# Kernel optimization log

Measured on AMD Instinct MI355X. Metric: run time of the kernel, lower is better.

## Reference

```python
import jax, jax.numpy as jnp
import numpy as np

B, N, FD, HD, MD, FS, NM = 8, 64, 128, 256, 64, 80, 6
D = HD + MD  # 320: GNN/decoder operating dim (fixes dim bug in original)
H = W = 128

def _mlp2(x, W1, b1, W2, b2):
    return jax.nn.relu(jax.nn.relu(x @ W1 + b1) @ W2 + b2)

def _forward(object_features, object_attributes, perception_features, object_positions,
             enc_W1, enc_b1, enc_W2, enc_b2, conv1_W, conv1_b, conv2_W, conv2_b,
             edge_W1, edge_b1, edge_W2, edge_b2, gru_Wih, gru_Whh, gru_bih, gru_bhh,
             mode_W1, mode_b1, mode_W2, mode_b2, traj_W1, traj_b1, traj_W2, traj_b2):
    # object encoder: [B,N,FD+8] -> [B,N,HD]
    obj_in = jnp.concatenate([object_features, object_attributes], -1)
    emb = _mlp2(obj_in, enc_W1, enc_b1, enc_W2, enc_b2)
    # map encoder (original discards result via random sampler; kept for faithfulness)
    dn = ('NCHW', 'OIHW', 'NCHW')
    m = jax.nn.relu(jax.lax.conv_general_dilated(perception_features, conv1_W, (1, 1), 'SAME', dimension_numbers=dn) + conv1_b[None, :, None, None])
    m = jax.nn.relu(jax.lax.conv_general_dilated(m, conv2_W, (1, 1), 'SAME', dimension_numbers=dn) + conv2_b[None, :, None, None])
    # sample_map_at_positions returns randn in the original; fixed-seed equivalent
    sampled = jax.random.normal(jax.random.key(42), (B, N, MD), dtype=emb.dtype)
    ctx = jnp.concatenate([emb, sampled], -1)  # [B,N,D]
    # Social GNN, fully vectorized over the ego-node loop i:
    rel = object_positions[:, :, None, :] - object_positions[:, None, :, :]  # [B,N,N,2] = pos[i]-pos[j]
    ego = jnp.broadcast_to(ctx[:, :, None, :], (B, N, N, D))
    nbr = jnp.broadcast_to(ctx[:, None, :, :], (B, N, N, D))
    e = _mlp2(jnp.concatenate([ego, nbr, rel], -1), edge_W1, edge_b1, edge_W2, edge_b2)  # [B,N,N,D]
    mask = (1.0 - jnp.eye(N, dtype=e.dtype))[None, :, :, None]
    agg = (e * mask).sum(2) / (N - 1 + 1e-10)  # [B,N,D]
    # GRUCell(input=concat(ctx,agg), hidden=ctx), torch semantics
    x = jnp.concatenate([ctx, agg], -1)  # [B,N,2D]
    gi = x @ gru_Wih + gru_bih
    gh = ctx @ gru_Whh + gru_bhh
    ir, iz, inn = jnp.split(gi, 3, -1)
    hr, hz, hn = jnp.split(gh, 3, -1)
    r = jax.nn.sigmoid(ir + hr)
    z = jax.nn.sigmoid(iz + hz)
    n = jnp.tanh(inn + r * hn)
    h = (1.0 - z) * n + z * ctx  # [B,N,D]
    # multi-modal trajectory decoder
    mode_probs = jax.nn.softmax(jax.nn.relu(h @ mode_W1 + mode_b1) @ mode_W2 + mode_b2, -1)  # [B,N,NM]
    t = jax.nn.relu(jnp.einsum('bnd,mde->bnme', h, traj_W1) + traj_b1)  # [B,N,NM,D]
    traj = jnp.einsum('bnme,mef->bnmf', t, traj_W2) + traj_b2  # [B,N,NM,FS*2]
    traj = traj.reshape(B, N, NM, FS, 2)
    return traj, mode_probs

def setup_inputs() -> dict:
    key = jax.random.key(0)
    ks = jax.random.split(key, 24)
    p = lambda k, shape: jax.random.normal(k, shape, dtype=jnp.float32) * 0.02
    z = lambda *shape: jnp.zeros(shape, dtype=jnp.float32)
    return {
        'object_features': jax.random.normal(ks[0], (B, N, FD), dtype=jnp.float32),
        'object_attributes': jax.random.normal(ks[1], (B, N, 8), dtype=jnp.float32),
        'perception_features': jax.random.normal(ks[2], (B, 256, H, W), dtype=jnp.float32),
        'object_positions': jax.random.normal(ks[3], (B, N, 2), dtype=jnp.float32),
        'enc_W1': p(ks[4], (FD + 8, HD)), 'enc_b1': z(HD),
        'enc_W2': p(ks[5], (HD, HD)), 'enc_b2': z(HD),
        'conv1_W': p(ks[6], (128, 256, 3, 3)), 'conv1_b': z(128),
        'conv2_W': p(ks[7], (64, 128, 3, 3)), 'conv2_b': z(64),
        'edge_W1': p(ks[8], (2 * D + 2, D)), 'edge_b1': z(D),
        'edge_W2': p(ks[9], (D, D)), 'edge_b2': z(D),
        'gru_Wih': p(ks[10], (2 * D, 3 * D)), 'gru_Whh': p(ks[11], (D, 3 * D)),
        'gru_bih': z(3 * D), 'gru_bhh': z(3 * D),
        'mode_W1': p(ks[12], (D, D)), 'mode_b1': z(D),
        'mode_W2': p(ks[13], (D, NM)), 'mode_b2': z(NM),
        'traj_W1': p(ks[14], (NM, D, D)), 'traj_b1': z(NM, D),
        'traj_W2': p(ks[15], (NM, D, FS * 2)), 'traj_b2': z(NM, FS * 2),
    }

def reference(object_features, object_attributes, perception_features, object_positions,
              enc_W1, enc_b1, enc_W2, enc_b2, conv1_W, conv1_b, conv2_W, conv2_b,
              edge_W1, edge_b1, edge_W2, edge_b2, gru_Wih, gru_Whh, gru_bih, gru_bhh,
              mode_W1, mode_b1, mode_W2, mode_b2, traj_W1, traj_b1, traj_W2, traj_b2):
    return _forward(object_features, object_attributes, perception_features, object_positions,
                    enc_W1, enc_b1, enc_W2, enc_b2, conv1_W, conv1_b, conv2_W, conv2_b,
                    edge_W1, edge_b1, edge_W2, edge_b2, gru_Wih, gru_Whh, gru_bih, gru_bhh,
                    mode_W1, mode_b1, mode_W2, mode_b2, traj_W1, traj_b1, traj_W2, traj_b2)
```

## Files before the change

### kernel.cpp

```cpp
#include <hip/hip_runtime.h>


typedef __attribute__((ext_vector_type(8))) short bf16x8;
typedef __attribute__((ext_vector_type(4))) float f32x4;

__device__ __forceinline__ unsigned short f2bf(float x) {
  unsigned u = __float_as_uint(x);
  return (unsigned short)((u + 0x7fffu + ((u >> 16) & 1u)) >> 16);
}

__device__ __forceinline__ void threefry2x32(unsigned k0, unsigned k1,
                                             unsigned& x0, unsigned& x1) {
  const unsigned ks0 = k0, ks1 = k1, ks2 = k0 ^ k1 ^ 0x1BD11BDAu;
  x0 += ks0; x1 += ks1;
#define TFR(r) { x0 += x1; x1 = (x1 << (r)) | (x1 >> (32 - (r))); x1 ^= x0; }
  TFR(13) TFR(15) TFR(26) TFR(6)  x0 += ks1; x1 += ks2 + 1u;
  TFR(17) TFR(29) TFR(16) TFR(24) x0 += ks2; x1 += ks0 + 2u;
  TFR(13) TFR(15) TFR(26) TFR(6)  x0 += ks0; x1 += ks1 + 3u;
  TFR(17) TFR(29) TFR(16) TFR(24) x0 += ks1; x1 += ks2 + 4u;
  TFR(13) TFR(15) TFR(26) TFR(6)  x0 += ks2; x1 += ks0 + 5u;
#undef TFR
}

__device__ __forceinline__ float erfinv_xla(float x) {
  float w = -logf((1.0f - x) * (1.0f + x));
  float p;
  if (w < 5.0f) {
    w = w - 2.5f;
    p = 2.81022636e-08f;
    p = fmaf(p, w, 3.43273939e-07f);
    p = fmaf(p, w, -3.5233877e-06f);
    p = fmaf(p, w, -4.39150654e-06f);
    p = fmaf(p, w, 0.00021858087f);
    p = fmaf(p, w, -0.00125372503f);
    p = fmaf(p, w, -0.00417768164f);
    p = fmaf(p, w, 0.246640727f);
    p = fmaf(p, w, 1.50140941f);
  } else {
    w = sqrtf(w) - 3.0f;
    p = -0.000200214257f;
    p = fmaf(p, w, 0.000100950558f);
    p = fmaf(p, w, 0.00134934322f);
    p = fmaf(p, w, -0.00367342844f);
    p = fmaf(p, w, 0.00573950773f);
    p = fmaf(p, w, -0.0076224613f);
    p = fmaf(p, w, 0.00943887047f);
    p = fmaf(p, w, 1.00167406f);
    p = fmaf(p, w, 2.83297682f);
  }
  return p * x;
}

__device__ __forceinline__ float jax_normal42(unsigned idx) {
  unsigned x0 = 0u, x1 = idx;
  threefry2x32(0u, 42u, x0, x1);
  unsigned bits = x0 ^ x1;
  float f = __uint_as_float((bits >> 9) | 0x3f800000u) - 1.0f;
  const float lo = -0.99999994f;
  float u = fmaxf(lo, f * 2.0f + lo);
  return 1.41421356237f * erfinv_xla(u);
}

__global__ __launch_bounds__(256)
void k_head(const float* __restrict__ W2e, const float* __restrict__ Wih,
            const float* __restrict__ Whh, const float* __restrict__ T1,
            const float* __restrict__ T2, const float* __restrict__ EW1,
            const float* __restrict__ MW1, const float* __restrict__ MW2,
            unsigned short* __restrict__ ub,
            const float* __restrict__ feat, const float* __restrict__ attr,
            const float* __restrict__ eW1, const float* __restrict__ eb1,
            const float* __restrict__ eW2, const float* __restrict__ eb2,
            float* __restrict__ ctx) {
  __shared__ float s_in[4][136];
  __shared__ float s_h1[4][256];
  const int t = threadIdx.x;

  if (blockIdx.x < 1103) {
    const int id = blockIdx.x * 256 + t;
    if (id >= 282240) return;
    if (id >= 281600) {
      const int rem = id - 281600;
      const int g = rem >> 4, n = rem & 15;
      unsigned short v[8];
#pragma unroll
      for (int e = 0; e < 8; ++e) v[e] = (n < 6) ? f2bf(MW2[(g * 8 + e) * 6 + n]) : 0;
      ushort4* d = (ushort4*)&ub[2252800 + (size_t)rem * 8];
      d[0] = make_ushort4(v[0], v[1], v[2], v[3]);
      d[1] = make_ushort4(v[4], v[5], v[6], v[7]);
      return;
    }
    const float* src;
    unsigned short* dst;
    int rem, N;
    if (id < 12800)       { src = W2e; dst = ub;           rem = id;          N = 320; }
    else if (id < 89600)  { src = Wih; dst = ub + 102400;  rem = id - 12800;  N = 960; }
    else if (id < 128000) { src = Whh; dst = ub + 716800;  rem = id - 89600;  N = 960; }
    else if (id < 204800) { src = T1;  dst = ub + 1024000; rem = id - 128000; N = 320; }
    else if (id < 243200) { src = T2;  dst = ub + 1638400; rem = id - 204800; N = 160; }
    else if (id < 268800) { src = EW1; dst = ub + 1945600; rem = id - 243200; N = 320; }
    else                  { src = MW1; dst = ub + 2150400; rem = id - 268800; N = 320; }
    const int g = rem / N, n = rem - g * N;
    const float* s = src + g * 8 * N + n;
    unsigned short v[8];
#pragma unroll
    for (int e = 0; e < 8; ++e) v[e] = f2bf(s[e * N]);
    ushort4* d = (ushort4*)&dst[(size_t)rem * 8];
    d[0] = make_ushort4(v[0], v[1], v[2], v[3]);
    d[1] = make_ushort4(v[4], v[5], v[6], v[7]);
    return;
  }

  const int r0 = (blockIdx.x - 1103) * 4;
  for (int r = 0; r < 4; ++r) {
    if (t < 128)      s_in[r][t] = feat[(r0 + r) * 128 + t];
    else if (t < 136) s_in[r][t] = attr[(r0 + r) * 8 + (t - 128)];
  }
  __syncthreads();
  float acc[4];
#pragma unroll
  for (int r = 0; r < 4; ++r) acc[r] = eb1[t];
  for (int k = 0; k < 136; ++k) {
    const float w = eW1[k * 256 + t];
#pragma unroll
    for (int r = 0; r < 4; ++r) acc[r] = fmaf(s_in[r][k], w, acc[r]);
  }
#pragma unroll
  for (int r = 0; r < 4; ++r) s_h1[r][t] = fmaxf(acc[r], 0.0f);
  __syncthreads();
#pragma unroll
  for (int r = 0; r < 4; ++r) acc[r] = eb2[t];
  for (int k = 0; k < 256; ++k) {
    const float w = eW2[k * 256 + t];
#pragma unroll
    for (int r = 0; r < 4; ++r) acc[r] = fmaf(s_h1[r][k], w, acc[r]);
  }
#pragma unroll
  for (int r = 0; r < 4; ++r) ctx[(r0 + r) * 320 + t] = fmaxf(acc[r], 0.0f);
  if (t < 64) {
    for (int r = 0; r < 4; ++r)
      ctx[(r0 + r) * 320 + 256 + t] = jax_normal42((unsigned)((r0 + r) * 64 + t));
  }
}

__global__ __launch_bounds__(256)
void k_pqM(const float* __restrict__ ctx, const unsigned short* __restrict__ Bf,
           const float* __restrict__ b1, float* __restrict__ P,
           float* __restrict__ Q) {
  __shared__ __align__(16) unsigned short s_c[40 * 16 * 8];
  const int row0 = blockIdx.x * 16;
  const int half = blockIdx.y;
  const int t = threadIdx.x;
#pragma unroll
  for (int it = 0; it < 3; ++it) {
    const int idx = t + it * 256;
    if (idx < 640) {
      const int row = idx / 40, oct = idx - row * 40;
      const float4 v0 = *(const float4*)&ctx[(row0 + row) * 320 + oct * 8];
      const float4 v1 = *(const float4*)&ctx[(row0 + row) * 320 + oct * 8 + 4];
      ushort4* dst = (ushort4*)&s_c[(oct * 16 + row) * 8];
      dst[0] = make_ushort4(f2bf(v0.x), f2bf(v0.y), f2bf(v0.z), f2bf(v0.w));
      dst[1] = make_ushort4(f2bf(v1.x), f2bf(v1.y), f2bf(v1.z), f2bf(v1.w));
    }
  }
  __syncthreads();

  const int w = t >> 6, l = t & 63, lg = l >> 4, lr = l & 15;
  f32x4 acc[5];
#pragma unroll
  for (int u = 0; u < 5; ++u) acc[u] = (f32x4){0.f, 0.f, 0.f, 0.f};
#pragma unroll
  for (int ks = 0; ks < 10; ++ks) {
    const bf16x8 afr = *(const bf16x8*)&s_c[((ks * 4 + lg) * 16 + lr) * 8];
    bf16x8 bfr[5];
#pragma unroll
    for (int u = 0; u < 5; ++u)
      bfr[u] = *(const bf16x8*)&Bf[(((ks * 4 + lg) * 640) + half * 320 +
                                    w * 80 + u * 16 + lr) * 8];
#pragma unroll
    for (int u = 0; u < 5; ++u)
      acc[u] = __builtin_amdgcn_mfma_f32_16x16x32_bf16(afr, bfr[u], acc[u], 0, 0, 0);
  }
#pragma unroll
  for (int u = 0; u < 5; ++u) {
    const int n = w * 80 + u * 16 + lr;
    const float bias = (half == 0) ? b1[n] : 0.0f;
    float* dst = (half == 0) ? P : Q;
#pragma unroll
    for (int r = 0; r < 4; ++r) {
      const int row = row0 + lg * 4 + r;
      dst[row * 320 + n] = acc[u][r] + bias;
    }
  }
}

__global__ __launch_bounds__(256)
void k_edge(const float* __restrict__ P, const float* __restrict__ Q,
            const float* __restrict__ pos, const float* __restrict__ W1,
            const unsigned short* __restrict__ Bf, const float* __restrict__ b2,
            float* __restrict__ agg) {
  __shared__ __align__(16) unsigned short s_A[40 * 64 * 8];
  const int bx = blockIdx.x;
  const int b = bx >> 6, i = bx & 63;
  const int t = threadIdx.x;
  const int w = t >> 6, l = t & 63;

  {
    const float2 pi = *(const float2*)&pos[b * 128 + 2 * i];
    const float* __restrict__ Prow = P + bx * 320;
    const float* __restrict__ w0 = W1 + 640 * 320;
    const float* __restrict__ w1 = W1 + 641 * 320;
#pragma unroll
    for (int it = 0; it < 10; ++it) {
      const int tau = w * 640 + it * 64 + l;
      const int j = tau / 40;
      const int oct = tau - j * 40;
      const int k0 = oct * 8;
      const float2 pj = *(const float2*)&pos[b * 128 + 2 * j];
      const float rx = pi.x - pj.x, ry = pi.y - pj.y;
      const float* __restrict__ Qrow = Q + (b * 64 + j) * 320;
      const float4 q0 = *(const float4*)&Qrow[k0];
      const float4 q1 = *(const float4*)&Qrow[k0 + 4];
      const float4 p0 = *(const float4*)&Prow[k0];
      const float4 p1 = *(const float4*)&Prow[k0 + 4];
      const float4 a0 = *(const float4*)&w0[k0];
      const float4 a1 = *(const float4*)&w0[k0 + 4];
      const float4 c0 = *(const float4*)&w1[k0];
      const float4 c1 = *(const float4*)&w1[k0 + 4];
      float v[8];
      v[0] = fmaf(ry, c0.x, fmaf(rx, a0.x, p0.x + q0.x));
      v[1] = fmaf(ry, c0.y, fmaf(rx, a0.y, p0.y + q0.y));
      v[2] = fmaf(ry, c0.z, fmaf(rx, a0.z, p0.z + q0.z));
      v[3] = fmaf(ry, c0.w, fmaf(rx, a0.w, p0.w + q0.w));
      v[4] = fmaf(ry, c1.x, fmaf(rx, a1.x, p1.x + q1.x));
      v[5] = fmaf(ry, c1.y, fmaf(rx, a1.y, p1.y + q1.y));
      v[6] = fmaf(ry, c1.z, fmaf(rx, a1.z, p1.z + q1.z));
      v[7] = fmaf(ry, c1.w, fmaf(rx, a1.w, p1.w + q1.w));
      unsigned short u[8];
#pragma unroll
      for (int e = 0; e < 8; ++e) u[e] = f2bf(fmaxf(v[e], 0.0f));
      const int swz = ((oct * 64 + j) * 8) ^ ((oct & 7) << 3);
      *(ushort4*)&s_A[swz]     = make_ushort4(u[0], u[1], u[2], u[3]);
      *(ushort4*)&s_A[swz + 4] = make_ushort4(u[4], u[5], u[6], u[7]);
    }
  }
  __syncthreads();

  f32x4 acc[4][5];
#pragma unroll
  for (int mt = 0; mt < 4; ++mt)
#pragma unroll
    for (int u = 0; u < 5; ++u) acc[mt][u] = (f32x4){0.f, 0.f, 0.f, 0.f};

  const int lg = l >> 4, lr = l & 15;
  const unsigned short* __restrict__ Bbase = Bf + (lg * 320 + w * 80 + lr) * 8;

#pragma unroll 2
  for (int ks = 0; ks < 10; ++ks) {
    const int oct = ks * 4 + lg;
    bf16x8 afr[4];
#pragma unroll
    for (int mt = 0; mt < 4; ++mt) {
      const int elem = ((oct * 64 + mt * 16 + lr) * 8) ^ ((oct & 7) << 3);
      afr[mt] = *(const bf16x8*)&s_A[elem];
    }
    bf16x8 bfr[5];
#pragma unroll
    for (int u = 0; u < 5; ++u)
      bfr[u] = *(const bf16x8*)(Bbase + ks * 10240 + u * 128);
#pragma unroll
    for (int mt = 0; mt < 4; ++mt)
#pragma unroll
      for (int u = 0; u < 5; ++u)
        acc[mt][u] = __builtin_amdgcn_mfma_f32_16x16x32_bf16(
            afr[mt], bfr[u], acc[mt][u], 0, 0, 0);
  }

#pragma unroll
  for (int u = 0; u < 5; ++u) {
    const int n = w * 80 + u * 16 + lr;
    const float bias = b2[n];
    float p = 0.0f;
#pragma unroll
    for (int mt = 0; mt < 4; ++mt) {
#pragma unroll
      for (int r = 0; r < 4; ++r) {
        const int j = mt * 16 + lg * 4 + r;
        const float e = fmaxf(acc[mt][u][r] + bias, 0.0f);
        p += (j != i) ? e : 0.0f;
      }
    }
    p += __shfl_xor(p, 16);
    p += __shfl_xor(p, 32);
    if (l < 16) agg[bx * 320 + n] = p * (1.0f / 63.0f);
  }
}

__global__ __launch_bounds__(256)
void k_gruM(const float* __restrict__ ctx, const float* __restrict__ agg,
            const unsigned short* __restrict__ BfI,
            const unsigned short* __restrict__ BfH,
            const float* __restrict__ bih, const float* __restrict__ bhh,
            float* __restrict__ h) {
  __shared__ __align__(16) unsigned short s_x[80 * 16 * 8];
  const int rb = blockIdx.x / 5, db = blockIdx.x % 5;
  const int row0 = rb * 16, d0 = db * 64;
  const int t = threadIdx.x;

#pragma unroll
  for (int it = 0; it < 5; ++it) {
    const int idx = t + it * 256;
    const int row = idx / 80, oct = idx - row * 80;
    float4 v0, v1;
    if (oct < 40) {
      v0 = *(const float4*)&ctx[(row0 + row) * 320 + oct * 8];
      v1 = *(const float4*)&ctx[(row0 + row) * 320 + oct * 8 + 4];
    } else {
      v0 = *(const float4*)&agg[(row0 + row) * 320 + (oct - 40) * 8];
      v1 = *(const float4*)&agg[(row0 + row) * 320 + (oct - 40) * 8 + 4];
    }
    ushort4* dst = (ushort4*)&s_x[(oct * 16 + row) * 8];
    dst[0] = make_ushort4(f2bf(v0.x), f2bf(v0.y), f2bf(v0.z), f2bf(v0.w));
    dst[1] = make_ushort4(f2bf(v1.x), f2bf(v1.y), f2bf(v1.z), f2bf(v1.w));
  }
  __syncthreads();

  const int w = t >> 6, l = t & 63, lg = l >> 4, lr = l & 15;
  const int d = d0 + w * 16 + lr;

  f32x4 accI[3], accH[3];
#pragma unroll
  for (int g = 0; g < 3; ++g) {
    accI[g] = (f32x4){0.f, 0.f, 0.f, 0.f};
    accH[g] = (f32x4){0.f, 0.f, 0.f, 0.f};
  }

#pragma unroll 2
  for (int ks = 0; ks < 20; ++ks) {
    const bf16x8 afr = *(const bf16x8*)&s_x[((ks * 4 + lg) * 16 + lr) * 8];
    bf16x8 bfr[3];
#pragma unroll
    for (int g = 0; g < 3; ++g)
      bfr[g] = *(const bf16x8*)&BfI[((ks * 4 + lg) * 960 + g * 320 + d) * 8];
#pragma unroll
    for (int g = 0; g < 3; ++g)
      accI[g] = __builtin_amdgcn_mfma_f32_16x16x32_bf16(afr, bfr[g], accI[g], 0, 0, 0);
  }
#pragma unroll 2
  for (int ks = 0; ks < 10; ++ks) {
    const bf16x8 afr = *(const bf16x8*)&s_x[((ks * 4 + lg) * 16 + lr) * 8];
    bf16x8 bfr[3];
#pragma unroll
    for (int g = 0; g < 3; ++g)
      bfr[g] = *(const bf16x8*)&BfH[((ks * 4 + lg) * 960 + g * 320 + d) * 8];
#pragma unroll
    for (int g = 0; g < 3; ++g)
      accH[g] = __builtin_amdgcn_mfma_f32_16x16x32_bf16(afr, bfr[g], accH[g], 0, 0, 0);
  }

  const float b_ir = bih[d], b_iz = bih[320 + d], b_in = bih[640 + d];
  const float b_hr = bhh[d], b_hz = bhh[320 + d], b_hn = bhh[640 + d];
#pragma unroll
  for (int r = 0; r < 4; ++r) {
    const int row = row0 + lg * 4 + r;
    const float ir = accI[0][r] + b_ir;
    const float iz = accI[1][r] + b_iz;
    const float inn = accI[2][r] + b_in;
    const float hr = accH[0][r] + b_hr;
    const float hz = accH[1][r] + b_hz;
    const float hn = accH[2][r] + b_hn;
    const float rr = 1.0f / (1.0f + expf(-(ir + hr)));
    const float zz = 1.0f / (1.0f + expf(-(iz + hz)));
    const float nn = tanhf(fmaf(rr, hn, inn));
    const float c = ctx[row * 320 + d];
    h[row * 320 + d] = (1.0f - zz) * nn + zz * c;
  }
}

__global__ __launch_bounds__(256)
void k_tail(const float* __restrict__ h, const unsigned short* __restrict__ MB1,
            const float* __restrict__ mb1, const unsigned short* __restrict__ MB2,
            const float* __restrict__ mb2, const unsigned short* __restrict__ TB1,
            const float* __restrict__ tb1, const unsigned short* __restrict__ TB2,
            const float* __restrict__ tb2, float* __restrict__ out) {
  __shared__ __align__(16) unsigned short s_buf[20480];
  __shared__ float s_l[32][6];
  const int t = threadIdx.x;
  const int w = t >> 6, l = t & 63, lg = l >> 4, lr = l & 15;

  if (blockIdx.x < 16) {
    unsigned short* s_h = s_buf;
    unsigned short* s_t = s_buf + 10240;
    const int row0 = blockIdx.x * 32;
#pragma unroll
    for (int it = 0; it < 5; ++it) {
      const int idx = t + it * 256;
      const int row = idx / 40, oct = idx - row * 40;
      const float4 v0 = *(const float4*)&h[(row0 + row) * 320 + oct * 8];
      const float4 v1 = *(const float4*)&h[(row0 + row) * 320 + oct * 8 + 4];
      ushort4* dst = (ushort4*)&s_h[(oct * 32 + row) * 8];
      dst[0] = make_ushort4(f2bf(v0.x), f2bf(v0.y), f2bf(v0.z), f2bf(v0.w));
      dst[1] = make_ushort4(f2bf(v1.x), f2bf(v1.y), f2bf(v1.z), f2bf(v1.w));
    }
    __syncthreads();

    f32x4 acc1[2][5];
#pragma unroll
    for (int mt = 0; mt < 2; ++mt)
#pragma unroll
      for (int u = 0; u < 5; ++u) acc1[mt][u] = (f32x4){0.f, 0.f, 0.f, 0.f};
#pragma unroll
    for (int ks = 0; ks < 10; ++ks) {
      bf16x8 afr[2];
#pragma unroll
      for (int mt = 0; mt < 2; ++mt)
        afr[mt] = *(const bf16x8*)&s_h[(((ks * 4 + lg) * 32) + mt * 16 + lr) * 8];
      bf16x8 bfr[5];
#pragma unroll
      for (int u = 0; u < 5; ++u)
        bfr[u] = *(const bf16x8*)&MB1[((ks * 4 + lg) * 320 + w * 80 + u * 16 + lr) * 8];
#pragma unroll
      for (int mt = 0; mt < 2; ++mt)
#pragma unroll
        for (int u = 0; u < 5; ++u)
          acc1[mt][u] = __builtin_amdgcn_mfma_f32_16x16x32_bf16(
              afr[mt], bfr[u], acc1[mt][u], 0, 0, 0);
    }
#pragma unroll
    for (int u = 0; u < 5; ++u) {
      const int n = w * 80 + u * 16 + lr;
      const float bias = mb1[n];
#pragma unroll
      for (int mt = 0; mt < 2; ++mt) {
#pragma unroll
        for (int r = 0; r < 4; ++r) {
          const int row = mt * 16 + lg * 4 + r;
          s_t[((n >> 3) * 32 + row) * 8 + (n & 7)] =
              f2bf(fmaxf(acc1[mt][u][r] + bias, 0.0f));
        }
      }
    }
    __syncthreads();

    if (w < 2) {
      f32x4 acc2 = (f32x4){0.f, 0.f, 0.f, 0.f};
#pragma unroll
      for (int ks = 0; ks < 10; ++ks) {
        const bf16x8 afr = *(const bf16x8*)&s_t[(((ks * 4 + lg) * 32) + w * 16 + lr) * 8];
        const bf16x8 bfr = *(const bf16x8*)&MB2[((ks * 4 + lg) * 16 + lr) * 8];
        acc2 = __builtin_amdgcn_mfma_f32_16x16x32_bf16(afr, bfr, acc2, 0, 0, 0);
      }
      if (lr < 6) {
#pragma unroll
        for (int r = 0; r < 4; ++r)
          s_l[w * 16 + lg * 4 + r][lr] = acc2[r] + mb2[lr];
      }
    }
    __syncthreads();

    if (t < 32) {
      float v[6];
#pragma unroll
      for (int q = 0; q < 6; ++q) v[q] = s_l[t][q];
      float mx = v[0];
#pragma unroll
      for (int q = 1; q < 6; ++q) mx = fmaxf(mx, v[q]);
      float sum = 0.0f;
#pragma unroll
      for (int q = 0; q < 6; ++q) { v[q] = expf(v[q] - mx); sum += v[q]; }
      const float inv = 1.0f / sum;
#pragma unroll
      for (int q = 0; q < 6; ++q) out[491520 + (row0 + t) * 6 + q] = v[q] * inv;
    }
    return;
  }

  const int idx0 = blockIdx.x - 16;
  const int m = idx0 >> 5, rb = idx0 & 31;
  unsigned short* s_h = s_buf;
  unsigned short* s_t = s_buf + 5120;
  const int row0 = rb * 16;

#pragma unroll
  for (int it = 0; it < 3; ++it) {
    const int idx = t + it * 256;
    if (idx < 640) {
      const int row = idx / 40, oct = idx - row * 40;
      const float4 v0 = *(const float4*)&h[(row0 + row) * 320 + oct * 8];
      const float4 v1 = *(const float4*)&h[(row0 + row) * 320 + oct * 8 + 4];
      ushort4* dst = (ushort4*)&s_h[(oct * 16 + row) * 8];
      dst[0] = make_ushort4(f2bf(v0.x), f2bf(v0.y), f2bf(v0.z), f2bf(v0.w));
      dst[1] = make_ushort4(f2bf(v1.x), f2bf(v1.y), f2bf(v1.z), f2bf(v1.w));
    }
  }
  __syncthreads();

  f32x4 acc1[5];
#pragma unroll
  for (int u = 0; u < 5; ++u) acc1[u] = (f32x4){0.f, 0.f, 0.f, 0.f};
  const unsigned short* __restrict__ B1m = TB1 + m * 102400;
#pragma unroll
  for (int ks = 0; ks < 10; ++ks) {
    const bf16x8 afr = *(const bf16x8*)&s_h[((ks * 4 + lg) * 16 + lr) * 8];
    bf16x8 bfr[5];
#pragma unroll
    for (int u = 0; u < 5; ++u)
      bfr[u] = *(const bf16x8*)&B1m[((ks * 4 + lg) * 320 + w * 80 + u * 16 + lr) * 8];
#pragma unroll
    for (int u = 0; u < 5; ++u)
      acc1[u] = __builtin_amdgcn_mfma_f32_16x16x32_bf16(afr, bfr[u], acc1[u], 0, 0, 0);
  }
#pragma unroll
  for (int u = 0; u < 5; ++u) {
    const int n = w * 80 + u * 16 + lr;
    const float bias = tb1[m * 320 + n];
#pragma unroll
    for (int r = 0; r < 4; ++r) {
      const int row = lg * 4 + r;
      s_t[((n >> 3) * 16 + row) * 8 + (n & 7)] =
          f2bf(fmaxf(acc1[u][r] + bias, 0.0f));
    }
  }
  __syncthreads();

  const int nb = (w == 0) ? 0 : (w == 1) ? 3 : (w == 2) ? 6 : 7;
  f32x4 acc2[3];
#pragma unroll
  for (int u = 0; u < 3; ++u) acc2[u] = (f32x4){0.f, 0.f, 0.f, 0.f};
  const unsigned short* __restrict__ B2m = TB2 + m * 51200;
#pragma unroll
  for (int ks = 0; ks < 10; ++ks) {
    const bf16x8 afr = *(const bf16x8*)&s_t[((ks * 4 + lg) * 16 + lr) * 8];
    bf16x8 bfr[3];
#pragma unroll
    for (int u = 0; u < 3; ++u)
      bfr[u] = *(const bf16x8*)&B2m[((ks * 4 + lg) * 160 + (nb + u) * 16 + lr) * 8];
#pragma unroll
    for (int u = 0; u < 3; ++u)
      acc2[u] = __builtin_amdgcn_mfma_f32_16x16x32_bf16(afr, bfr[u], acc2[u], 0, 0, 0);
  }
#pragma unroll
  for (int u = 0; u < 3; ++u) {
    const int n = (nb + u) * 16 + lr;
    const float bias = tb2[m * 160 + n];
#pragma unroll
    for (int r = 0; r < 4; ++r) {
      const int row = row0 + lg * 4 + r;
      out[(row * 6 + m) * 160 + n] = acc2[u][r] + bias;
    }
  }
}

extern "C" void kernel_launch(void* const* d_in, const int* in_sizes, int n_in,
                              void* d_out, int out_size, void* d_ws, size_t ws_size,
                              hipStream_t stream) {
  (void)in_sizes; (void)n_in; (void)out_size; (void)ws_size;
  const float* feat  = (const float*)d_in[0];
  const float* attr  = (const float*)d_in[1];
  const float* pos   = (const float*)d_in[3];
  const float* encW1 = (const float*)d_in[4];
  const float* encb1 = (const float*)d_in[5];
  const float* encW2 = (const float*)d_in[6];
  const float* encb2 = (const float*)d_in[7];
  const float* edgW1 = (const float*)d_in[12];
  const float* edgb1 = (const float*)d_in[13];
  const float* edgW2 = (const float*)d_in[14];
  const float* edgb2 = (const float*)d_in[15];
  const float* Wih   = (const float*)d_in[16];
  const float* Whh   = (const float*)d_in[17];
  const float* bih   = (const float*)d_in[18];
  const float* bhh   = (const float*)d_in[19];
  const float* mW1   = (const float*)d_in[20];
  const float* mb1   = (const float*)d_in[21];
  const float* mW2   = (const float*)d_in[22];
  const float* mb2   = (const float*)d_in[23];
  const float* tW1   = (const float*)d_in[24];
  const float* tb1   = (const float*)d_in[25];
  const float* tW2   = (const float*)d_in[26];
  const float* tb2   = (const float*)d_in[27];

  float* out = (float*)d_out;
  float* ws  = (float*)d_ws;
  float* ctx  = ws;
  float* P    = ws + 163840;
  float* Q    = ws + 327680;
  float* agg  = ws + 491520;
  float* hbuf = ws + 655360;
  unsigned short* ub = (unsigned short*)(ws + 819200);
  unsigned short* W2bf  = ub;
  unsigned short* WihBf = ub + 102400;
  unsigned short* WhhBf = ub + 716800;
  unsigned short* T1bf  = ub + 1024000;
  unsigned short* T2bf  = ub + 1638400;
  unsigned short* EW1bf = ub + 1945600;
  unsigned short* MW1bf = ub + 2150400;
  unsigned short* MW2bf = ub + 2252800;

  k_head<<<1231, 256, 0, stream>>>(edgW2, Wih, Whh, tW1, tW2, edgW1, mW1, mW2, ub,
                                   feat, attr, encW1, encb1, encW2, encb2, ctx);
  k_pqM<<<dim3(32, 2), 256, 0, stream>>>(ctx, EW1bf, edgb1, P, Q);
  k_edge<<<512, 256, 0, stream>>>(P, Q, pos, edgW1, W2bf, edgb2, agg);
  k_gruM<<<160, 256, 0, stream>>>(ctx, agg, WihBf, WhhBf, bih, bhh, hbuf);
  k_tail<<<208, 256, 0, stream>>>(hbuf, MW1bf, mb1, MW2bf, mb2,
                                  T1bf, tb1, T2bf, tb2, out);
}
```

Baseline: 78.35 us.

## Fuse all stages into one persistent kernel with software grid barriers

Merges the five kernel launches into a single 256-block persistent kernel, with stages separated by an atomic-counter grid barrier, and adds a memset to reset the barrier. This removes per-launch overhead and the gaps between launches. In exchange, each stage now runs on at most 256 blocks, so the weight conversion and edge work loop over more items per block. The barrier spin-waits also add cost, and the scheme assumes all 256 blocks are co-resident.

```diff
diff --git a/kernel.cpp b/kernel.cpp
--- a/kernel.cpp
+++ b/kernel.cpp
@@ -61,23 +61,55 @@
   return 1.41421356237f * erfinv_xla(u);
 }
 
+__device__ __forceinline__ void gridbar(unsigned* bar, unsigned target) {
+  __syncthreads();
+  if (threadIdx.x == 0) {
+    __threadfence();
+    if (atomicAdd(&bar[0], 1u) == 255u) {
+      bar[0] = 0u;
+      __threadfence();
+      atomicAdd(&bar[1], 1u);
+    } else {
+      while (atomicAdd(&bar[1], 0u) < target) { __builtin_amdgcn_s_sleep(2); }
+    }
+    __threadfence();
+  }
+  __syncthreads();
+}
+
 __global__ __launch_bounds__(256)
-void k_head(const float* __restrict__ W2e, const float* __restrict__ Wih,
-            const float* __restrict__ Whh, const float* __restrict__ T1,
-            const float* __restrict__ T2, const float* __restrict__ EW1,
-            const float* __restrict__ MW1, const float* __restrict__ MW2,
-            unsigned short* __restrict__ ub,
-            const float* __restrict__ feat, const float* __restrict__ attr,
-            const float* __restrict__ eW1, const float* __restrict__ eb1,
-            const float* __restrict__ eW2, const float* __restrict__ eb2,
-            float* __restrict__ ctx) {
-  __shared__ float s_in[4][136];
-  __shared__ float s_h1[4][256];
+void k_fused(const float* __restrict__ W2e, const float* __restrict__ Wih,
+             const float* __restrict__ Whh, const float* __restrict__ T1,
+             const float* __restrict__ T2, const float* __restrict__ EW1,
+             const float* __restrict__ MW1, const float* __restrict__ MW2,
+             unsigned short* __restrict__ ub,
+             const float* __restrict__ feat, const float* __restrict__ attr,
+             const float* __restrict__ eW1, const float* __restrict__ eb1,
+             const float* __restrict__ eW2, const float* __restrict__ eb2,
+             const float* __restrict__ pos, const float* __restrict__ edgW1,
+             const float* __restrict__ edgb1, const float* __restrict__ edgb2,
+             const float* __restrict__ bih, const float* __restrict__ bhh,
+             const float* __restrict__ mb1, const float* __restrict__ mb2,
+             const float* __restrict__ tb1, const float* __restrict__ tb2,
+             float* __restrict__ ctx, float* __restrict__ P,
+             float* __restrict__ Q, float* __restrict__ agg,
+             float* __restrict__ hbuf, float* __restrict__ out,
+             unsigned* __restrict__ bar) {
+  __shared__ __align__(16) unsigned char smem[41728];
+  const int bid = blockIdx.x;
   const int t = threadIdx.x;
-
-  if (blockIdx.x < 1103) {
-    const int id = blockIdx.x * 256 + t;
-    if (id >= 282240) return;
+  const int w = t >> 6, l = t & 63, lg = (l >> 4), lr = l & 15;
+
+  const unsigned short* W2bf  = ub;
+  const unsigned short* WihBf = ub + 102400;
+  const unsigned short* WhhBf = ub + 716800;
+  const unsigned short* T1bf  = ub + 1024000;
+  const unsigned short* T2bf  = ub + 1638400;
+  const unsigned short* EW1bf = ub + 1945600;
+  const unsigned short* MW1bf = ub + 2150400;
+  const unsigned short* MW2bf = ub + 2252800;
+
+  for (int id = bid * 256 + t; id < 282240; id += 65536) {
     if (id >= 281600) {
       const int rem = id - 281600;
       const int g = rem >> 4, n = rem & 15;
@@ -87,7 +119,7 @@
       ushort4* d = (ushort4*)&ub[2252800 + (size_t)rem * 8];
       d[0] = make_ushort4(v[0], v[1], v[2], v[3]);
       d[1] = make_ushort4(v[4], v[5], v[6], v[7]);
-      return;
+      continue;
     }
     const float* src;
     unsigned short* dst;
@@ -107,296 +139,268 @@
     ushort4* d = (ushort4*)&dst[(size_t)rem * 8];
     d[0] = make_ushort4(v[0], v[1], v[2], v[3]);
     d[1] = make_ushort4(v[4], v[5], v[6], v[7]);
-    return;
-  }
-
-  const int r0 = (blockIdx.x - 1103) * 4;
-  for (int r = 0; r < 4; ++r) {
-    if (t < 128)      s_in[r][t] = feat[(r0 + r) * 128 + t];
-    else if (t < 136) s_in[r][t] = attr[(r0 + r) * 8 + (t - 128)];
-  }
-  __syncthreads();
-  float acc[4];
-#pragma unroll
-  for (int r = 0; r < 4; ++r) acc[r] = eb1[t];
-  for (int k = 0; k < 136; ++k) {
-    const float w = eW1[k * 256 + t];
-#pragma unroll
-    for (int r = 0; r < 4; ++r) acc[r] = fmaf(s_in[r][k], w, acc[r]);
-  }
-#pragma unroll
-  for (int r = 0; r < 4; ++r) s_h1[r][t] = fmaxf(acc[r], 0.0f);
-  __syncthreads();
-#pragma unroll
-  for (int r = 0; r < 4; ++r) acc[r] = eb2[t];
-  for (int k = 0; k < 256; ++k) {
-    const float w = eW2[k * 256 + t];
-#pragma unroll
-    for (int r = 0; r < 4; ++r) acc[r] = fmaf(s_h1[r][k], w, acc[r]);
-  }
-#pragma unroll
-  for (int r = 0; r < 4; ++r) ctx[(r0 + r) * 320 + t] = fmaxf(acc[r], 0.0f);
-  if (t < 64) {
-    for (int r = 0; r < 4; ++r)
-      ctx[(r0 + r) * 320 + 256 + t] = jax_normal42((unsigned)((r0 + r) * 64 + t));
-  }
-}
-
-__global__ __launch_bounds__(256)
-void k_pqM(const float* __restrict__ ctx, const unsigned short* __restrict__ Bf,
-           const float* __restrict__ b1, float* __restrict__ P,
-           float* __restrict__ Q) {
-  __shared__ __align__(16) unsigned short s_c[40 * 16 * 8];
-  const int row0 = blockIdx.x * 16;
-  const int half = blockIdx.y;
-  const int t = threadIdx.x;
-#pragma unroll
-  for (int it = 0; it < 3; ++it) {
-    const int idx = t + it * 256;
-    if (idx < 640) {
-      const int row = idx / 40, oct = idx - row * 40;
-      const float4 v0 = *(const float4*)&ctx[(row0 + row) * 320 + oct * 8];
-      const float4 v1 = *(const float4*)&ctx[(row0 + row) * 320 + oct * 8 + 4];
-      ushort4* dst = (ushort4*)&s_c[(oct * 16 + row) * 8];
+  }
+
+  {
+    float (*s_in)[136] = (float (*)[136])smem;
+    float (*s_h1)[256] = (float (*)[256])(smem + 2 * 136 * 4);
+    const int r0 = bid * 2;
+    for (int r = 0; r < 2; ++r) {
+      if (t < 128)      s_in[r][t] = feat[(r0 + r) * 128 + t];
+      else if (t < 136) s_in[r][t] = attr[(r0 + r) * 8 + (t - 128)];
+    }
+    __syncthreads();
+    float acc[2];
+#pragma unroll
+    for (int r = 0; r < 2; ++r) acc[r] = eb1[t];
+    for (int k = 0; k < 136; ++k) {
+      const float ww = eW1[k * 256 + t];
+#pragma unroll
+      for (int r = 0; r < 2; ++r) acc[r] = fmaf(s_in[r][k], ww, acc[r]);
+    }
+#pragma unroll
+    for (int r = 0; r < 2; ++r) s_h1[r][t] = fmaxf(acc[r], 0.0f);
+    __syncthreads();
+#pragma unroll
+    for (int r = 0; r < 2; ++r) acc[r] = eb2[t];
+    for (int k = 0; k < 256; ++k) {
+      const float ww = eW2[k * 256 + t];
+#pragma unroll
+      for (int r = 0; r < 2; ++r) acc[r] = fmaf(s_h1[r][k], ww, acc[r]);
+    }
+#pragma unroll
+    for (int r = 0; r < 2; ++r) ctx[(r0 + r) * 320 + t] = fmaxf(acc[r], 0.0f);
+    if (t < 64) {
+      for (int r = 0; r < 2; ++r)
+        ctx[(r0 + r) * 320 + 256 + t] = jax_normal42((unsigned)((r0 + r) * 64 + t));
+    }
+  }
+  gridbar(bar, 1);
+
+  if (bid < 64) {
+    unsigned short* s_c = (unsigned short*)smem;
+    const int row0 = (bid >> 1) * 16;
+    const int half = bid & 1;
+#pragma unroll
+    for (int it = 0; it < 3; ++it) {
+      const int idx = t + it * 256;
+      if (idx < 640) {
+        const int row = idx / 40, oct = idx - row * 40;
+        const float4 v0 = *(const float4*)&ctx[(row0 + row) * 320 + oct * 8];
+        const float4 v1 = *(const float4*)&ctx[(row0 + row) * 320 + oct * 8 + 4];
+        ushort4* dst = (ushort4*)&s_c[(oct * 16 + row) * 8];
+        dst[0] = make_ushort4(f2bf(v0.x), f2bf(v0.y), f2bf(v0.z), f2bf(v0.w));
+        dst[1] = make_ushort4(f2bf(v1.x), f2bf(v1.y), f2bf(v1.z), f2bf(v1.w));
+      }
+    }
+    __syncthreads();
+    f32x4 acc[5];
+#pragma unroll
+    for (int u = 0; u < 5; ++u) acc[u] = (f32x4){0.f, 0.f, 0.f, 0.f};
+#pragma unroll
+    for (int ks = 0; ks < 10; ++ks) {
+      const bf16x8 afr = *(const bf16x8*)&s_c[((ks * 4 + lg) * 16 + lr) * 8];
+      bf16x8 bfr[5];
+#pragma unroll
+      for (int u = 0; u < 5; ++u)
+        bfr[u] = *(const bf16x8*)&EW1bf[(((ks * 4 + lg) * 640) + half * 320 +
+                                        w * 80 + u * 16 + lr) * 8];
+#pragma unroll
+      for (int u = 0; u < 5; ++u)
+        acc[u] = __builtin_amdgcn_mfma_f32_16x16x32_bf16(afr, bfr[u], acc[u], 0, 0, 0);
+    }
+#pragma unroll
+    for (int u = 0; u < 5; ++u) {
+      const int n = w * 80 + u * 16 + lr;
+      const float bias = (half == 0) ? edgb1[n] : 0.0f;
+      float* dst = (half == 0) ? P : Q;
+#pragma unroll
+      for (int r = 0; r < 4; ++r) {
+        const int row = row0 + lg * 4 + r;
+        dst[row * 320 + n] = acc[u][r] + bias;
+      }
+    }
+  }
+  gridbar(bar, 2);
+
+  {
+    unsigned short* s_A = (unsigned short*)smem;
+    for (int sub = 0; sub < 2; ++sub) {
+      const int bx = bid * 2 + sub;
+      const int b = bx >> 6, i = bx & 63;
+      {
+        const float2 pi = *(const float2*)&pos[b * 128 + 2 * i];
+        const float* __restrict__ Prow = P + bx * 320;
+        const float* __restrict__ w0 = edgW1 + 640 * 320;
+        const float* __restrict__ w1 = edgW1 + 641 * 320;
+#pragma unroll
+        for (int it = 0; it < 10; ++it) {
+          const int tau = w * 640 + it * 64 + l;
+          const int j = tau / 40;
+          const int oct = tau - j * 40;
+          const int k0 = oct * 8;
+          const float2 pj = *(const float2*)&pos[b * 128 + 2 * j];
+          const float rx = pi.x - pj.x, ry = pi.y - pj.y;
+          const float* __restrict__ Qrow = Q + (b * 64 + j) * 320;
+          const float4 q0 = *(const float4*)&Qrow[k0];
+          const float4 q1 = *(const float4*)&Qrow[k0 + 4];
+          const float4 p0 = *(const float4*)&Prow[k0];
+          const float4 p1 = *(const float4*)&Prow[k0 + 4];
+          const float4 a0 = *(const float4*)&w0[k0];
+          const float4 a1 = *(const float4*)&w0[k0 + 4];
+          const float4 c0 = *(const float4*)&w1[k0];
+          const float4 c1 = *(const float4*)&w1[k0 + 4];
+          float v[8];
+          v[0] = fmaf(ry, c0.x, fmaf(rx, a0.x, p0.x + q0.x));
+          v[1] = fmaf(ry, c0.y, fmaf(rx, a0.y, p0.y + q0.y));
+          v[2] = fmaf(ry, c0.z, fmaf(rx, a0.z, p0.z + q0.z));
+          v[3] = fmaf(ry, c0.w, fmaf(rx, a0.w, p0.w + q0.w));
+          v[4] = fmaf(ry, c1.x, fmaf(rx, a1.x, p1.x + q1.x));
+          v[5] = fmaf(ry, c1.y, fmaf(rx, a1.y, p1.y + q1.y));
+          v[6] = fmaf(ry, c1.z, fmaf(rx, a1.z, p1.z + q1.z));
+          v[7] = fmaf(ry, c1.w, fmaf(rx, a1.w, p1.w + q1.w));
+          unsigned short u[8];
+#pragma unroll
+          for (int e = 0; e < 8; ++e) u[e] = f2bf(fmaxf(v[e], 0.0f));
+          const int swz = ((oct * 64 + j) * 8) ^ ((oct & 7) << 3);
+          *(ushort4*)&s_A[swz]     = make_ushort4(u[0], u[1], u[2], u[3]);
+          *(ushort4*)&s_A[swz + 4] = make_ushort4(u[4], u[5], u[6], u[7]);
+        }
+      }
+      __syncthreads();
+
+      f32x4 acc[4][5];
+#pragma unroll
+      for (int mt = 0; mt < 4; ++mt)
+#pragma unroll
+        for (int u = 0; u < 5; ++u) acc[mt][u] = (f32x4){0.f, 0.f, 0.f, 0.f};
+      const unsigned short* __restrict__ Bbase = W2bf + (lg * 320 + w * 80 + lr) * 8;
+#pragma unroll 2
+      for (int ks = 0; ks < 10; ++ks) {
+        const int oct = ks * 4 + lg;
+        bf16x8 afr[4];
+#pragma unroll
+        for (int mt = 0; mt < 4; ++mt) {
+          const int elem = ((oct * 64 + mt * 16 + lr) * 8) ^ ((oct & 7) << 3);
+          afr[mt] = *(const bf16x8*)&s_A[elem];
+        }
+        bf16x8 bfr[5];
+#pragma unroll
+        for (int u = 0; u < 5; ++u)
+          bfr[u] = *(const bf16x8*)(Bbase + ks * 10240 + u * 128);
+#pragma unroll
+        for (int mt = 0; mt < 4; ++mt)
+#pragma unroll
+          for (int u = 0; u < 5; ++u)
+            acc[mt][u] = __builtin_amdgcn_mfma_f32_16x16x32_bf16(
+                afr[mt], bfr[u], acc[mt][u], 0, 0, 0);
+      }
+
+#pragma unroll
+      for (int u = 0; u < 5; ++u) {
+        const int n = w * 80 + u * 16 + lr;
+        const float bias = edgb2[n];
+        float p = 0.0f;
+#pragma unroll
+        for (int mt = 0; mt < 4; ++mt) {
+#pragma unroll
+          for (int r = 0; r < 4; ++r) {
+            const int j = mt * 16 + lg * 4 + r;
+            const float e = fmaxf(acc[mt][u][r] + bias, 0.0f);
+            p += (j != i) ? e : 0.0f;
+          }
+        }
+        p += __shfl_xor(p, 16);
+        p += __shfl_xor(p, 32);
+        if (l < 16) agg[bx * 320 + n] = p * (1.0f / 63.0f);
+      }
+      __syncthreads();
+    }
+  }
+  gridbar(bar, 3);
+
+  if (bid < 160) {
+    unsigned short* s_x = (unsigned short*)smem;
+    const int rb = bid / 5, db = bid % 5;
+    const int row0 = rb * 16, d0 = db * 64;
+#pragma unroll
+    for (int it = 0; it < 5; ++it) {
+      const int idx = t + it * 256;
+      const int row = idx / 80, oct = idx - row * 80;
+      float4 v0, v1;
+      if (oct < 40) {
+        v0 = *(const float4*)&ctx[(row0 + row) * 320 + oct * 8];
+        v1 = *(const float4*)&ctx[(row0 + row) * 320 + oct * 8 + 4];
+      } else {
+        v0 = *(const float4*)&agg[(row0 + row) * 320 + (oct - 40) * 8];
+        v1 = *(const float4*)&agg[(row0 + row) * 320 + (oct - 40) * 8 + 4];
+      }
+      ushort4* dst = (ushort4*)&s_x[(oct * 16 + row) * 8];
       dst[0] = make_ushort4(f2bf(v0.x), f2bf(v0.y), f2bf(v0.z), f2bf(v0.w));
       dst[1] = make_ushort4(f2bf(v1.x), f2bf(v1.y), f2bf(v1.z), f2bf(v1.w));
     }
-  }
-  __syncthreads();
-
-  const int w = t >> 6, l = t & 63, lg = l >> 4, lr = l & 15;
-  f32x4 acc[5];
-#pragma unroll
-  for (int u = 0; u < 5; ++u) acc[u] = (f32x4){0.f, 0.f, 0.f, 0.f};
-#pragma unroll
-  for (int ks = 0; ks < 10; ++ks) {
-    const bf16x8 afr = *(const bf16x8*)&s_c[((ks * 4 + lg) * 16 + lr) * 8];
-    bf16x8 bfr[5];
-#pragma unroll
-    for (int u = 0; u < 5; ++u)
-      bfr[u] = *(const bf16x8*)&Bf[(((ks * 4 + lg) * 640) + half * 320 +
-                                    w * 80 + u * 16 + lr) * 8];
-#pragma unroll
-    for (int u = 0; u < 5; ++u)
-      acc[u] = __builtin_amdgcn_mfma_f32_16x16x32_bf16(afr, bfr[u], acc[u], 0, 0, 0);
-  }
-#pragma unroll
-  for (int u = 0; u < 5; ++u) {
-    const int n = w * 80 + u * 16 + lr;
-    const float bias = (half == 0) ? b1[n] : 0.0f;
-    float* dst = (half == 0) ? P : Q;
+    __syncthreads();
+
+    const int d = d0 + w * 16 + lr;
+    f32x4 accI[3], accH[3];
+#pragma unroll
+    for (int g = 0; g < 3; ++g) {
+      accI[g] = (f32x4){0.f, 0.f, 0.f, 0.f};
+      accH[g] = (f32x4){0.f, 0.f, 0.f, 0.f};
+    }
+#pragma unroll 2
+    for (int ks = 0; ks < 20; ++ks) {
+      const bf16x8 afr = *(const bf16x8*)&s_x[((ks * 4 + lg) * 16 + lr) * 8];
+      bf16x8 bfr[3];
+#pragma unroll
+      for (int g = 0; g < 3; ++g)
+        bfr[g] = *(const bf16x8*)&WihBf[((ks * 4 + lg) * 960 + g * 320 + d) * 8];
+#pragma unroll
+      for (int g = 0; g < 3; ++g)
+        accI[g] = __builtin_amdgcn_mfma_f32_16x16x32_bf16(afr, bfr[g], accI[g], 0, 0, 0);
+    }
+#pragma unroll 2
+    for (int ks = 0; ks < 10; ++ks) {
+      const bf16x8 afr = *(const bf16x8*)&s_x[((ks * 4 + lg) * 16 + lr) * 8];
+      bf16x8 bfr[3];
+#pragma unroll
+      for (int g = 0; g < 3; ++g)
+        bfr[g] = *(const bf16x8*)&WhhBf[((ks * 4 + lg) * 960 + g * 320 + d) * 8];
+#pragma unroll
+      for (int g = 0; g < 3; ++g)
+        accH[g] = __builtin_amdgcn_mfma_f32_16x16x32_bf16(afr, bfr[g], accH[g], 0, 0, 0);
+    }
+    const float b_ir = bih[d], b_iz = bih[320 + d], b_in = bih[640 + d];
+    const float b_hr = bhh[d], b_hz = bhh[320 + d], b_hn = bhh[640 + d];
 #pragma unroll
     for (int r = 0; r < 4; ++r) {
       const int row = row0 + lg * 4 + r;
-      dst[row * 320 + n] = acc[u][r] + bias;
-    }
-  }
-}
-
-__global__ __launch_bounds__(256)
-void k_edge(const float* __restrict__ P, const float* __restrict__ Q,
-            const float* __restrict__ pos, const float* __restrict__ W1,
-            const unsigned short* __restrict__ Bf, const float* __restrict__ b2,
-            float* __restrict__ agg) {
-  __shared__ __align__(16) unsigned short s_A[40 * 64 * 8];
-  const int bx = blockIdx.x;
-  const int b = bx >> 6, i = bx & 63;
-  const int t = threadIdx.x;
-  const int w = t >> 6, l = t & 63;
-
-  {
-    const float2 pi = *(const float2*)&pos[b * 128 + 2 * i];
-    const float* __restrict__ Prow = P + bx * 320;
-    const float* __restrict__ w0 = W1 + 640 * 320;
-    const float* __restrict__ w1 = W1 + 641 * 320;
-#pragma unroll
-    for (int it = 0; it < 10; ++it) {
-      const int tau = w * 640 + it * 64 + l;
-      const int j = tau / 40;
-      const int oct = tau - j * 40;
-      const int k0 = oct * 8;
-      const float2 pj = *(const float2*)&pos[b * 128 + 2 * j];
-      const float rx = pi.x - pj.x, ry = pi.y - pj.y;
-      const float* __restrict__ Qrow = Q + (b * 64 + j) * 320;
-      const float4 q0 = *(const float4*)&Qrow[k0];
-      const float4 q1 = *(const float4*)&Qrow[k0 + 4];
-      const float4 p0 = *(const float4*)&Prow[k0];
-      const float4 p1 = *(const float4*)&Prow[k0 + 4];
-      const float4 a0 = *(const float4*)&w0[k0];
-      const float4 a1 = *(const float4*)&w0[k0 + 4];
-      const float4 c0 = *(const float4*)&w1[k0];
-      const float4 c1 = *(const float4*)&w1[k0 + 4];
-      float v[8];
-      v[0] = fmaf(ry, c0.x, fmaf(rx, a0.x, p0.x + q0.x));
-      v[1] = fmaf(ry, c0.y, fmaf(rx, a0.y, p0.y + q0.y));
-      v[2] = fmaf(ry, c0.z, fmaf(rx, a0.z, p0.z + q0.z));
-      v[3] = fmaf(ry, c0.w, fmaf(rx, a0.w, p0.w + q0.w));
-      v[4] = fmaf(ry, c1.x, fmaf(rx, a1.x, p1.x + q1.x));
-      v[5] = fmaf(ry, c1.y, fmaf(rx, a1.y, p1.y + q1.y));
-      v[6] = fmaf(ry, c1.z, fmaf(rx, a1.z, p1.z + q1.z));
-      v[7] = fmaf(ry, c1.w, fmaf(rx, a1.w, p1.w + q1.w));
-      unsigned short u[8];
-#pragma unroll
-      for (int e = 0; e < 8; ++e) u[e] = f2bf(fmaxf(v[e], 0.0f));
-      const int swz = ((oct * 64 + j) * 8) ^ ((oct & 7) << 3);
-      *(ushort4*)&s_A[swz]     = make_ushort4(u[0], u[1], u[2], u[3]);
-      *(ushort4*)&s_A[swz + 4] = make_ushort4(u[4], u[5], u[6], u[7]);
-    }
-  }
-  __syncthreads();
-
-  f32x4 acc[4][5];
-#pragma unroll
-  for (int mt = 0; mt < 4; ++mt)
-#pragma unroll
-    for (int u = 0; u < 5; ++u) acc[mt][u] = (f32x4){0.f, 0.f, 0.f, 0.f};
-
-  const int lg = l >> 4, lr = l & 15;
-  const unsigned short* __restrict__ Bbase = Bf + (lg * 320 + w * 80 + lr) * 8;
-
-#pragma unroll 2
-  for (int ks = 0; ks < 10; ++ks) {
-    const int oct = ks * 4 + lg;
-    bf16x8 afr[4];
-#pragma unroll
-    for (int mt = 0; mt < 4; ++mt) {
-      const int elem = ((oct * 64 + mt * 16 + lr) * 8) ^ ((oct & 7) << 3);
-      afr[mt] = *(const bf16x8*)&s_A[elem];
-    }
-    bf16x8 bfr[5];
-#pragma unroll
-    for (int u = 0; u < 5; ++u)
-      bfr[u] = *(const bf16x8*)(Bbase + ks * 10240 + u * 128);
-#pragma unroll
-    for (int mt = 0; mt < 4; ++mt)
-#pragma unroll
-      for (int u = 0; u < 5; ++u)
-        acc[mt][u] = __builtin_amdgcn_mfma_f32_16x16x32_bf16(
-            afr[mt], bfr[u], acc[mt][u], 0, 0, 0);
-  }
-
-#pragma unroll
-  for (int u = 0; u < 5; ++u) {
-    const int n = w * 80 + u * 16 + lr;
-    const float bias = b2[n];
-    float p = 0.0f;
-#pragma unroll
-    for (int mt = 0; mt < 4; ++mt) {
-#pragma unroll
-      for (int r = 0; r < 4; ++r) {
-        const int j = mt * 16 + lg * 4 + r;
-        const float e = fmaxf(acc[mt][u][r] + bias, 0.0f);
-        p += (j != i) ? e : 0.0f;
-      }
-    }
-    p += __shfl_xor(p, 16);
-    p += __shfl_xor(p, 32);
-    if (l < 16) agg[bx * 320 + n] = p * (1.0f / 63.0f);
-  }
-}
-
-__global__ __launch_bounds__(256)
-void k_gruM(const float* __restrict__ ctx, const float* __restrict__ agg,
-            const unsigned short* __restrict__ BfI,
-            const unsigned short* __restrict__ BfH,
-            const float* __restrict__ bih, const float* __restrict__ bhh,
-            float* __restrict__ h) {
-  __shared__ __align__(16) unsigned short s_x[80 * 16 * 8];
-  const int rb = blockIdx.x / 5, db = blockIdx.x % 5;
-  const int row0 = rb * 16, d0 = db * 64;
-  const int t = threadIdx.x;
-
-#pragma unroll
-  for (int it = 0; it < 5; ++it) {
-    const int idx = t + it * 256;
-    const int row = idx / 80, oct = idx - row * 80;
-    float4 v0, v1;
-    if (oct < 40) {
-      v0 = *(const float4*)&ctx[(row0 + row) * 320 + oct * 8];
-      v1 = *(const float4*)&ctx[(row0 + row) * 320 + oct * 8 + 4];
-    } else {
-      v0 = *(const float4*)&agg[(row0 + row) * 320 + (oct - 40) * 8];
-      v1 = *(const float4*)&agg[(row0 + row) * 320 + (oct - 40) * 8 + 4];
-    }
-    ushort4* dst = (ushort4*)&s_x[(oct * 16 + row) * 8];
-    dst[0] = make_ushort4(f2bf(v0.x), f2bf(v0.y), f2bf(v0.z), f2bf(v0.w));
-    dst[1] = make_ushort4(f2bf(v1.x), f2bf(v1.y), f2bf(v1.z), f2bf(v1.w));
-  }
-  __syncthreads();
-
-  const int w = t >> 6, l = t & 63, lg = l >> 4, lr = l & 15;
-  const int d = d0 + w * 16 + lr;
-
-  f32x4 accI[3], accH[3];
-#pragma unroll
-  for (int g = 0; g < 3; ++g) {
-    accI[g] = (f32x4){0.f, 0.f, 0.f, 0.f};
-    accH[g] = (f32x4){0.f, 0.f, 0.f, 0.f};
-  }
-
-#pragma unroll 2
-  for (int ks = 0; ks < 20; ++ks) {
-    const bf16x8 afr = *(const bf16x8*)&s_x[((ks * 4 + lg) * 16 + lr) * 8];
-    bf16x8 bfr[3];
-#pragma unroll
-    for (int g = 0; g < 3; ++g)
-      bfr[g] = *(const bf16x8*)&BfI[((ks * 4 + lg) * 960 + g * 320 + d) * 8];
-#pragma unroll
-    for (int g = 0; g < 3; ++g)
-      accI[g] = __builtin_amdgcn_mfma_f32_16x16x32_bf16(afr, bfr[g], accI[g], 0, 0, 0);
-  }
-#pragma unroll 2
-  for (int ks = 0; ks < 10; ++ks) {
-    const bf16x8 afr = *(const bf16x8*)&s_x[((ks * 4 + lg) * 16 + lr) * 8];
-    bf16x8 bfr[3];
-#pragma unroll
-    for (int g = 0; g < 3; ++g)
-      bfr[g] = *(const bf16x8*)&BfH[((ks * 4 + lg) * 960 + g * 320 + d) * 8];
-#pragma unroll
-    for (int g = 0; g < 3; ++g)
-      accH[g] = __builtin_amdgcn_mfma_f32_16x16x32_bf16(afr, bfr[g], accH[g], 0, 0, 0);
-  }
-
-  const float b_ir = bih[d], b_iz = bih[320 + d], b_in = bih[640 + d];
-  const float b_hr = bhh[d], b_hz = bhh[320 + d], b_hn = bhh[640 + d];
-#pragma unroll
-  for (int r = 0; r < 4; ++r) {
-    const int row = row0 + lg * 4 + r;
-    const float ir = accI[0][r] + b_ir;
-    const float iz = accI[1][r] + b_iz;
-    const float inn = accI[2][r] + b_in;
-    const float hr = accH[0][r] + b_hr;
-    const float hz = accH[1][r] + b_hz;
-    const float hn = accH[2][r] + b_hn;
-    const float rr = 1.0f / (1.0f + expf(-(ir + hr)));
-    const float zz = 1.0f / (1.0f + expf(-(iz + hz)));
-    const float nn = tanhf(fmaf(rr, hn, inn));
-    const float c = ctx[row * 320 + d];
-    h[row * 320 + d] = (1.0f - zz) * nn + zz * c;
-  }
-}
-
-__global__ __launch_bounds__(256)
-void k_tail(const float* __restrict__ h, const unsigned short* __restrict__ MB1,
-            const float* __restrict__ mb1, const unsigned short* __restrict__ MB2,
-            const float* __restrict__ mb2, const unsigned short* __restrict__ TB1,
-            const float* __restrict__ tb1, const unsigned short* __restrict__ TB2,
-            const float* __restrict__ tb2, float* __restrict__ out) {
-  __shared__ __align__(16) unsigned short s_buf[20480];
-  __shared__ float s_l[32][6];
-  const int t = threadIdx.x;
-  const int w = t >> 6, l = t & 63, lg = l >> 4, lr = l & 15;
-
-  if (blockIdx.x < 16) {
-    unsigned short* s_h = s_buf;
-    unsigned short* s_t = s_buf + 10240;
-    const int row0 = blockIdx.x * 32;
+      const float ir = accI[0][r] + b_ir;
+      const float iz = accI[1][r] + b_iz;
+      const float inn = accI[2][r] + b_in;
+      const float hr = accH[0][r] + b_hr;
+      const float hz = accH[1][r] + b_hz;
+      const float hn = accH[2][r] + b_hn;
+      const float rr = 1.0f / (1.0f + expf(-(ir + hr)));
+      const float zz = 1.0f / (1.0f + expf(-(iz + hz)));
+      const float nn = tanhf(fmaf(rr, hn, inn));
+      const float c = ctx[row * 320 + d];
+      hbuf[row * 320 + d] = (1.0f - zz) * nn + zz * c;
+    }
+  }
+  gridbar(bar, 4);
+
+  if (bid < 16) {
+    unsigned short* s_h = (unsigned short*)smem;
+    unsigned short* s_t = (unsigned short*)(smem + 20480);
+    float (*s_l)[6] = (float (*)[6])(smem + 40960);
+    const int row0 = bid * 32;
 #pragma unroll
     for (int it = 0; it < 5; ++it) {
       const int idx = t + it * 256;
       const int row = idx / 40, oct = idx - row * 40;
-      const float4 v0 = *(const float4*)&h[(row0 + row) * 320 + oct * 8];
-      const float4 v1 = *(const float4*)&h[(row0 + row) * 320 + oct * 8 + 4];
+      const float4 v0 = *(const float4*)&hbuf[(row0 + row) * 320 + oct * 8];
+      const float4 v1 = *(const float4*)&hbuf[(row0 + row) * 320 + oct * 8 + 4];
       ushort4* dst = (ushort4*)&s_h[(oct * 32 + row) * 8];
       dst[0] = make_ushort4(f2bf(v0.x), f2bf(v0.y), f2bf(v0.z), f2bf(v0.w));
       dst[1] = make_ushort4(f2bf(v1.x), f2bf(v1.y), f2bf(v1.z), f2bf(v1.w));
@@ -417,7 +421,7 @@
       bf16x8 bfr[5];
 #pragma unroll
       for (int u = 0; u < 5; ++u)
-        bfr[u] = *(const bf16x8*)&MB1[((ks * 4 + lg) * 320 + w * 80 + u * 16 + lr) * 8];
+        bfr[u] = *(const bf16x8*)&MW1bf[((ks * 4 + lg) * 320 + w * 80 + u * 16 + lr) * 8];
 #pragma unroll
       for (int mt = 0; mt < 2; ++mt)
 #pragma unroll
@@ -446,7 +450,7 @@
 #pragma unroll
       for (int ks = 0; ks < 10; ++ks) {
         const bf16x8 afr = *(const bf16x8*)&s_t[(((ks * 4 + lg) * 32) + w * 16 + lr) * 8];
-        const bf16x8 bfr = *(const bf16x8*)&MB2[((ks * 4 + lg) * 16 + lr) * 8];
+        const bf16x8 bfr = *(const bf16x8*)&MW2bf[((ks * 4 + lg) * 16 + lr) * 8];
         acc2 = __builtin_amdgcn_mfma_f32_16x16x32_bf16(afr, bfr, acc2, 0, 0, 0);
       }
       if (lr < 6) {
@@ -471,81 +475,79 @@
 #pragma unroll
       for (int q = 0; q < 6; ++q) out[491520 + (row0 + t) * 6 + q] = v[q] * inv;
     }
-    return;
-  }
-
-  const int idx0 = blockIdx.x - 16;
-  const int m = idx0 >> 5, rb = idx0 & 31;
-  unsigned short* s_h = s_buf;
-  unsigned short* s_t = s_buf + 5120;
-  const int row0 = rb * 16;
-
-#pragma unroll
-  for (int it = 0; it < 3; ++it) {
-    const int idx = t + it * 256;
-    if (idx < 640) {
-      const int row = idx / 40, oct = idx - row * 40;
-      const float4 v0 = *(const float4*)&h[(row0 + row) * 320 + oct * 8];
-      const float4 v1 = *(const float4*)&h[(row0 + row) * 320 + oct * 8 + 4];
-      ushort4* dst = (ushort4*)&s_h[(oct * 16 + row) * 8];
-      dst[0] = make_ushort4(f2bf(v0.x), f2bf(v0.y), f2bf(v0.z), f2bf(v0.w));
-      dst[1] = make_ushort4(f2bf(v1.x), f2bf(v1.y), f2bf(v1.z), f2bf(v1.w));
-    }
-  }
-  __syncthreads();
-
-  f32x4 acc1[5];
-#pragma unroll
-  for (int u = 0; u < 5; ++u) acc1[u] = (f32x4){0.f, 0.f, 0.f, 0.f};
-  const unsigned short* __restrict__ B1m = TB1 + m * 102400;
-#pragma unroll
-  for (int ks = 0; ks < 10; ++ks) {
-    const bf16x8 afr = *(const bf16x8*)&s_h[((ks * 4 + lg) * 16 + lr) * 8];
-    bf16x8 bfr[5];
-#pragma unroll
-    for (int u = 0; u < 5; ++u)
-      bfr[u] = *(const bf16x8*)&B1m[((ks * 4 + lg) * 320 + w * 80 + u * 16 + lr) * 8];
-#pragma unroll
-    for (int u = 0; u < 5; ++u)
-      acc1[u] = __builtin_amdgcn_mfma_f32_16x16x32_bf16(afr, bfr[u], acc1[u], 0, 0, 0);
-  }
-#pragma unroll
-  for (int u = 0; u < 5; ++u) {
-    const int n = w * 80 + u * 16 + lr;
-    const float bias = tb1[m * 320 + n];
-#pragma unroll
-    for (int r = 0; r < 4; ++r) {
-      const int row = lg * 4 + r;
-      s_t[((n >> 3) * 16 + row) * 8 + (n & 7)] =
-          f2bf(fmaxf(acc1[u][r] + bias, 0.0f));
-    }
-  }
-  __syncthreads();
-
-  const int nb = (w == 0) ? 0 : (w == 1) ? 3 : (w == 2) ? 6 : 7;
-  f32x4 acc2[3];
-#pragma unroll
-  for (int u = 0; u < 3; ++u) acc2[u] = (f32x4){0.f, 0.f, 0.f, 0.f};
-  const unsigned short* __restrict__ B2m = TB2 + m * 51200;
-#pragma unroll
-  for (int ks = 0; ks < 10; ++ks) {
-    const bf16x8 afr = *(const bf16x8*)&s_t[((ks * 4 + lg) * 16 + lr) * 8];
-    bf16x8 bfr[3];
-#pragma unroll
-    for (int u = 0; u < 3; ++u)
-      bfr[u] = *(const bf16x8*)&B2m[((ks * 4 + lg) * 160 + (nb + u) * 16 + lr) * 8];
-#pragma unroll
-    for (int u = 0; u < 3; ++u)
-      acc2[u] = __builtin_amdgcn_mfma_f32_16x16x32_bf16(afr, bfr[u], acc2[u], 0, 0, 0);
-  }
-#pragma unroll
-  for (int u = 0; u < 3; ++u) {
-    const int n = (nb + u) * 16 + lr;
-    const float bias = tb2[m * 160 + n];
-#pragma unroll
-    for (int r = 0; r < 4; ++r) {
-      const int row = row0 + lg * 4 + r;
-      out[(row * 6 + m) * 160 + n] = acc2[u][r] + bias;
+  } else if (bid < 208) {
+    const int idx0 = bid - 16;
+    const int m = idx0 >> 5, rb = idx0 & 31;
+    unsigned short* s_h = (unsigned short*)smem;
+    unsigned short* s_t = (unsigned short*)(smem + 10240);
+    const int row0 = rb * 16;
+#pragma unroll
+    for (int it = 0; it < 3; ++it) {
+      const int idx = t + it * 256;
+      if (idx < 640) {
+        const int row = idx / 40, oct = idx - row * 40;
+        const float4 v0 = *(const float4*)&hbuf[(row0 + row) * 320 + oct * 8];
+        const float4 v1 = *(const float4*)&hbuf[(row0 + row) * 320 + oct * 8 + 4];
+        ushort4* dst = (ushort4*)&s_h[(oct * 16 + row) * 8];
+        dst[0] = make_ushort4(f2bf(v0.x), f2bf(v0.y), f2bf(v0.z), f2bf(v0.w));
+        dst[1] = make_ushort4(f2bf(v1.x), f2bf(v1.y), f2bf(v1.z), f2bf(v1.w));
+      }
+    }
+    __syncthreads();
+
+    f32x4 acc1[5];
+#pragma unroll
+    for (int u = 0; u < 5; ++u) acc1[u] = (f32x4){0.f, 0.f, 0.f, 0.f};
+    const unsigned short* __restrict__ B1m = T1bf + m * 102400;
+#pragma unroll
+    for (int ks = 0; ks < 10; ++ks) {
+      const bf16x8 afr = *(const bf16x8*)&s_h[((ks * 4 + lg) * 16 + lr) * 8];
+      bf16x8 bfr[5];
+#pragma unroll
+      for (int u = 0; u < 5; ++u)
+        bfr[u] = *(const bf16x8*)&B1m[((ks * 4 + lg) * 320 + w * 80 + u * 16 + lr) * 8];
+#pragma unroll
+      for (int u = 0; u < 5; ++u)
+        acc1[u] = __builtin_amdgcn_mfma_f32_16x16x32_bf16(afr, bfr[u], acc1[u], 0, 0, 0);
+    }
+#pragma unroll
+    for (int u = 0; u < 5; ++u) {
+      const int n = w * 80 + u * 16 + lr;
+      const float bias = tb1[m * 320 + n];
+#pragma unroll
+      for (int r = 0; r < 4; ++r) {
+        const int row = lg * 4 + r;
+        s_t[((n >> 3) * 16 + row) * 8 + (n & 7)] =
+            f2bf(fmaxf(acc1[u][r] + bias, 0.0f));
+      }
+    }
+    __syncthreads();
+
+    const int nb = (w == 0) ? 0 : (w == 1) ? 3 : (w == 2) ? 6 : 7;
+    f32x4 acc2[3];
+#pragma unroll
+    for (int u = 0; u < 3; ++u) acc2[u] = (f32x4){0.f, 0.f, 0.f, 0.f};
+    const unsigned short* __restrict__ B2m = T2bf + m * 51200;
+#pragma unroll
+    for (int ks = 0; ks < 10; ++ks) {
+      const bf16x8 afr = *(const bf16x8*)&s_t[((ks * 4 + lg) * 16 + lr) * 8];
+      bf16x8 bfr[3];
+#pragma unroll
+      for (int u = 0; u < 3; ++u)
+        bfr[u] = *(const bf16x8*)&B2m[((ks * 4 + lg) * 160 + (nb + u) * 16 + lr) * 8];
+#pragma unroll
+      for (int u = 0; u < 3; ++u)
+        acc2[u] = __builtin_amdgcn_mfma_f32_16x16x32_bf16(afr, bfr[u], acc2[u], 0, 0, 0);
+    }
+#pragma unroll
+    for (int u = 0; u < 3; ++u) {
+      const int n = (nb + u) * 16 + lr;
+      const float bias = tb2[m * 160 + n];
+#pragma unroll
+      for (int r = 0; r < 4; ++r) {
+        const int row = row0 + lg * 4 + r;
+        out[(row * 6 + m) * 160 + n] = acc2[u][r] + bias;
+      }
     }
   }
 }
@@ -586,20 +588,12 @@
   float* agg  = ws + 491520;
   float* hbuf = ws + 655360;
   unsigned short* ub = (unsigned short*)(ws + 819200);
-  unsigned short* W2bf  = ub;
-  unsigned short* WihBf = ub + 102400;
-  unsigned short* WhhBf = ub + 716800;
-  unsigned short* T1bf  = ub + 1024000;
-  unsigned short* T2bf  = ub + 1638400;
-  unsigned short* EW1bf = ub + 1945600;
-  unsigned short* MW1bf = ub + 2150400;
-  unsigned short* MW2bf = ub + 2252800;
-
-  k_head<<<1231, 256, 0, stream>>>(edgW2, Wih, Whh, tW1, tW2, edgW1, mW1, mW2, ub,
-                                   feat, attr, encW1, encb1, encW2, encb2, ctx);
-  k_pqM<<<dim3(32, 2), 256, 0, stream>>>(ctx, EW1bf, edgb1, P, Q);
-  k_edge<<<512, 256, 0, stream>>>(P, Q, pos, edgW1, W2bf, edgb2, agg);
-  k_gruM<<<160, 256, 0, stream>>>(ctx, agg, WihBf, WhhBf, bih, bhh, hbuf);
-  k_tail<<<208, 256, 0, stream>>>(hbuf, MW1bf, mb1, MW2bf, mb2,
-                                  T1bf, tb1, T2bf, tb2, out);
-}
+  unsigned* bar = (unsigned*)(ws + 1948160);
+
+  hipMemsetAsync((void*)bar, 0, 16, stream);
+  k_fused<<<256, 256, 0, stream>>>(
+      edgW2, Wih, Whh, tW1, tW2, edgW1, mW1, mW2, ub,
+      feat, attr, encW1, encb1, encW2, encb2,
+      pos, edgW1, edgb1, edgb2, bih, bhh, mb1, mb2, tb1, tb2,
+      ctx, P, Q, agg, hbuf, out, bar);
+}
```

Result: slower. 141.6 us (+80.7%).
